# Performance work log

Measured on AMD Instinct MI355X. Metric: run time of the kernel, lower is better.

The kernel has to match this reference:

```python
import jax, jax.numpy as jnp
import numpy as np

B, INPUT_LEN, F_IN = 32, 4096, 256
N = B * INPUT_LEN          # 131072 total nodes in the flattened batch
E = 4_194_304              # ~avg degree 32
HID, OUT = 3, 1            # GCNConv(256->3) then GCNConv(3->1), per source code
PRED_LEN = 1024


def setup_inputs() -> dict:
    key = jax.random.key(0)
    k = jax.random.split(key, 5)
    node_features = jax.random.normal(k[0], (B, INPUT_LEN, F_IN), dtype=jnp.float32)
    # flattened, already-offset edge index (Batch.from_data_list result)
    edge_index = jax.random.randint(k[1], (2, E), 0, N, dtype=jnp.int32)
    W1 = jax.random.normal(k[2], (F_IN, HID), dtype=jnp.float32) / np.float32(np.sqrt(F_IN))
    b1 = jnp.zeros((HID,), dtype=jnp.float32)
    W2 = jax.random.normal(k[3], (HID, OUT), dtype=jnp.float32) / np.float32(np.sqrt(HID))
    b2 = jnp.zeros((OUT,), dtype=jnp.float32)
    return {"node_features": node_features, "W1": W1, "b1": b1, "W2": W2, "b2": b2,
            "edge_index": edge_index, "pred_len": PRED_LEN, "input_len": INPUT_LEN}


def _gcn_norm(edge_index, num_nodes, dtype):
    # PyG gcn_norm: add self-loops, deg over destination, symmetric deg^-1/2 norm
    loop = jnp.arange(num_nodes, dtype=edge_index.dtype)
    src = jnp.concatenate([edge_index[0], loop])
    dst = jnp.concatenate([edge_index[1], loop])
    deg = jax.ops.segment_sum(jnp.ones_like(src, dtype=dtype), dst, num_segments=num_nodes)
    dinv = jnp.where(deg > 0, jax.lax.rsqrt(deg), 0.0).astype(dtype)
    norm = dinv[src] * dinv[dst]  # [E+N]
    return src, dst, norm


def _gcn_conv(x, src, dst, norm, W, b, num_nodes):
    h = x @ W                              # [N, out] linear first (small out dim)
    msg = h[src] * norm[:, None]           # gather + scale per edge
    out = jax.ops.segment_sum(msg, dst, num_segments=num_nodes)  # scatter-add
    return out + b


def reference(node_features, W1, b1, W2, b2, edge_index, pred_len, input_len):
    n_nodes = node_features.shape[0] * node_features.shape[1]
    x = node_features.reshape(n_nodes, node_features.shape[2])
    src, dst, norm = _gcn_norm(edge_index, n_nodes, x.dtype)
    h = jax.nn.relu(_gcn_conv(x, src, dst, norm, W1, b1, n_nodes))
    h = _gcn_conv(h, src, dst, norm, W2, b2, n_nodes)
    h = h.reshape(-1, input_len, h.shape[1])   # [B, input_len, num_target]
    return h[:, :pred_len, :]
```

## Files before the change

### kernel.cpp

```cpp
#include <hip/hip_runtime.h>
#include <hip/hip_bf16.h>
#include <stdint.h>

#define F_IN 256
#define QSCALE 512.0f
#define QBIAS  8192
#define FMASK  0x1FFFFFull
#define H2Q    16384.0f
#define NBUK   16
#define BCAP   524288
#define LCAP   384
#define XBUF_SZ  (32u << 20)
#define DEGSTG_OFF (32u << 20)
#define STG1_OFF   (34u << 20)
#define STG2_OFF   (50u << 20)
#define SCRATCH_SZ (52u << 20)

__device__ __forceinline__ float bf2f(unsigned short u) {
    union { unsigned int i; float f; } v; v.i = ((unsigned int)u) << 16; return v.f;
}
__device__ __forceinline__ unsigned short f2bf(float f) {
    union { unsigned int i; float f; } v; v.f = f;
    unsigned int r = v.i + 0x7FFF + ((v.i >> 16) & 1);
    return (unsigned short)(r >> 16);
}
__device__ __forceinline__ unsigned long long packq(float v0, float v1, float v2) {
    int m0 = __float2int_rn(v0 * QSCALE);
    int m1 = __float2int_rn(v1 * QSCALE);
    int m2 = __float2int_rn(v2 * QSCALE);
    m0 = max(-4095, min(4095, m0));
    m1 = max(-4095, min(4095, m1));
    m2 = max(-4095, min(4095, m2));
    return (unsigned long long)(unsigned)(m0 + QBIAS)
         | ((unsigned long long)(unsigned)(m1 + QBIAS) << 21)
         | ((unsigned long long)(unsigned)(m2 + QBIAS) << 42);
}

__global__ void k_init(unsigned int* __restrict__ gcur,
                       const unsigned int* __restrict__ w1w, int* __restrict__ flag) {
    __shared__ int cnt;
    if (threadIdx.x == 0) cnt = 0;
    if (threadIdx.x < NBUK) gcur[threadIdx.x] = 0u;
    __syncthreads();
    int local = 0;
    for (int i = threadIdx.x; i < 384; i += blockDim.x) {
        unsigned e = (w1w[i] >> 7) & 0xFF;
        if (e >= 100 && e <= 135) local++;
    }
    atomicAdd(&cnt, local);
    __syncthreads();
    if (threadIdx.x == 0) *flag = (2 * cnt < 384) ? 1 : 0;
}

__global__ void __launch_bounds__(1024)
k_bucket(const int* __restrict__ src, const int* __restrict__ dst,
         unsigned int* __restrict__ xbuf, unsigned int* __restrict__ gcur, int E) {
    __shared__ unsigned int lbuf[NBUK][LCAP];
    __shared__ unsigned int lcnt[NBUK];
    __shared__ unsigned int lbase[NBUK];
    if (threadIdx.x < NBUK) lcnt[threadIdx.x] = 0u;
    __syncthreads();
    int g4 = blockIdx.x * 1024 + threadIdx.x;
    int4 s4 = ((const int4*)src)[g4];
    int4 d4 = ((const int4*)dst)[g4];
    #pragma unroll
    for (int u = 0; u < 4; u++) {
        int s = (u == 0) ? s4.x : (u == 1) ? s4.y : (u == 2) ? s4.z : s4.w;
        int d = (u == 0) ? d4.x : (u == 1) ? d4.y : (u == 2) ? d4.z : d4.w;
        unsigned p = ((unsigned)s << 13) | ((unsigned)d & 8191u);
        int bk = ((unsigned)d) >> 13;
        unsigned lp = atomicAdd(&lcnt[bk], 1u);
        if (lp < LCAP) lbuf[bk][lp] = p;
        else {
            unsigned g = atomicAdd(&gcur[bk], 1u);
            xbuf[(size_t)bk * BCAP + g] = p;
        }
    }
    __syncthreads();
    if (threadIdx.x < NBUK) {
        unsigned c = min(lcnt[threadIdx.x], (unsigned)LCAP);
        lcnt[threadIdx.x] = c;
        lbase[threadIdx.x] = atomicAdd(&gcur[threadIdx.x], c);
    }
    __syncthreads();
    for (int bk = 0; bk < NBUK; bk++) {
        unsigned c = lcnt[bk], base = lbase[bk];
        for (unsigned i = threadIdx.x; i < c; i += 1024)
            xbuf[(size_t)bk * BCAP + base + i] = lbuf[bk][i];
    }
}

__global__ void __launch_bounds__(1024)
k_gemv_bhist(int bhistB,
             const unsigned int* __restrict__ xbuf, const unsigned int* __restrict__ gcur,
             unsigned int* __restrict__ degstg,
             const void* __restrict__ xv_, const void* __restrict__ w1_,
             unsigned short* __restrict__ h1con,
             const int* __restrict__ flag, int N) {
    __shared__ unsigned int cnt8[2048];
    int b = blockIdx.x;
    if (b < bhistB) {
        int bucket = b & 15, sub = b >> 4;
        for (int i = threadIdx.x; i < 2048; i += 1024) cnt8[i] = 0u;
        __syncthreads();
        unsigned cnt = gcur[bucket];
        unsigned e0 = (unsigned)(((unsigned long long)sub       * cnt) >> 4);
        unsigned e1 = (unsigned)(((unsigned long long)(sub + 1) * cnt) >> 4);
        const unsigned int* bp = xbuf + (size_t)bucket * BCAP;
        for (unsigned i = e0 + threadIdx.x; i < e1; i += 1024) {
            unsigned q = bp[i] & 8191u;
            atomicAdd(&cnt8[q >> 2], 1u << ((q & 3u) << 3));
        }
        __syncthreads();
        unsigned int* out = degstg + (size_t)b * 2048;
        for (int i = threadIdx.x; i < 2048; i += 1024) out[i] = cnt8[i];
        return;
    }
    int wave = threadIdx.x >> 6;
    int lane = threadIdx.x & 63;
    int row0 = ((b - bhistB) * 16 + wave) * 2;
    if (row0 >= N) return;
    int f32mode = *flag;

    float xa0, xa1, xa2, xa3, xb0, xb1, xb2, xb3;
    float w00, w01, w02, w10, w11, w12, w20, w21, w22, w30, w31, w32;
    if (f32mode) {
        const float4* xra = (const float4*)((const float*)xv_ + (size_t)row0 * F_IN);
        const float4* xrb = (const float4*)((const float*)xv_ + (size_t)(row0 + 1) * F_IN);
        float4 va = xra[lane], vb = xrb[lane];
        xa0 = va.x; xa1 = va.y; xa2 = va.z; xa3 = va.w;
        xb0 = vb.x; xb1 = vb.y; xb2 = vb.z; xb3 = vb.w;
        const float4* wr = (const float4*)w1_;
        float4 wa = wr[lane*3+0], wb = wr[lane*3+1], wc = wr[lane*3+2];
        w00 = wa.x; w01 = wa.y; w02 = wa.z; w10 = wa.w;
        w11 = wb.x; w12 = wb.y; w20 = wb.z; w21 = wb.w;
        w22 = wc.x; w30 = wc.y; w31 = wc.z; w32 = wc.w;
    } else {
        const ushort4* xra = (const ushort4*)((const unsigned short*)xv_ + (size_t)row0 * F_IN);
        const ushort4* xrb = (const ushort4*)((const unsigned short*)xv_ + (size_t)(row0 + 1) * F_IN);
        ushort4 va = xra[lane], vb = xrb[lane];
        xa0 = bf2f(va.x); xa1 = bf2f(va.y); xa2 = bf2f(va.z); xa3 = bf2f(va.w);
        xb0 = bf2f(vb.x); xb1 = bf2f(vb.y); xb2 = bf2f(vb.z); xb3 = bf2f(vb.w);
        const ushort4* wr = (const ushort4*)w1_;
        ushort4 wa = wr[lane*3+0], wb = wr[lane*3+1], wc = wr[lane*3+2];
        w00 = bf2f(wa.x); w01 = bf2f(wa.y); w02 = bf2f(wa.z); w10 = bf2f(wa.w);
        w11 = bf2f(wb.x); w12 = bf2f(wb.y); w20 = bf2f(wb.z); w21 = bf2f(wb.w);
        w22 = bf2f(wc.x); w30 = bf2f(wc.y); w31 = bf2f(wc.z); w32 = bf2f(wc.w);
    }
    float pa0 = xa0*w00 + xa1*w10 + xa2*w20 + xa3*w30;
    float pa1 = xa0*w01 + xa1*w11 + xa2*w21 + xa3*w31;
    float pa2 = xa0*w02 + xa1*w12 + xa2*w22 + xa3*w32;
    float pb0 = xb0*w00 + xb1*w10 + xb2*w20 + xb3*w30;
    float pb1 = xb0*w01 + xb1*w11 + xb2*w21 + xb3*w31;
    float pb2 = xb0*w02 + xb1*w12 + xb2*w22 + xb3*w32;
    #pragma unroll
    for (int off = 32; off; off >>= 1) {
        pa0 += __shfl_down(pa0, off, 64);
        pa1 += __shfl_down(pa1, off, 64);
        pa2 += __shfl_down(pa2, off, 64);
        pb0 += __shfl_down(pb0, off, 64);
        pb1 += __shfl_down(pb1, off, 64);
        pb2 += __shfl_down(pb2, off, 64);
    }
    if (lane == 0) {
        ushort4 oa, ob;
        oa.x = f2bf(pa0); oa.y = f2bf(pa1); oa.z = f2bf(pa2); oa.w = 0;
        ob.x = f2bf(pb0); ob.y = f2bf(pb1); ob.z = f2bf(pb2); ob.w = 0;
        ((ushort4*)h1con)[row0]     = oa;
        ((ushort4*)h1con)[row0 + 1] = ob;
    }
}

__global__ void k_dinvpack(const unsigned char* __restrict__ degstg,
                           unsigned char* __restrict__ deg8, float* __restrict__ dinv,
                           unsigned long long* __restrict__ h1con, int N) {
    int n = blockIdx.x * blockDim.x + threadIdx.x;
    if (n >= N) return;
    int bk = n >> 13, idx = n & 8191;
    unsigned deg = 1u;
    #pragma unroll
    for (int s = 0; s < 16; s++)
        deg += degstg[(size_t)((s << 4) | bk) * 8192 + idx];
    deg8[n] = (unsigned char)deg;
    float dv = rsqrtf((float)deg);
    dinv[n] = dv;
    ushort4 h = ((const ushort4*)h1con)[n];
    h1con[n] = packq(bf2f(h.x) * dv, bf2f(h.y) * dv, bf2f(h.z) * dv);
}

__global__ void __launch_bounds__(1024)
k_scatter1(const unsigned int* __restrict__ xbuf,
           const unsigned long long* __restrict__ con,
           unsigned long long* __restrict__ stg1,
           const unsigned int* __restrict__ gcur) {
    __shared__ unsigned long long acc[8192];
    int bucket = blockIdx.x & 15, sub = blockIdx.x >> 4;
    for (int i = threadIdx.x; i < 8192; i += 1024) acc[i] = 0ull;
    __syncthreads();
    unsigned cnt = gcur[bucket];
    unsigned e0 = (unsigned)(((unsigned long long)sub       * cnt) >> 4);
    unsigned e1 = (unsigned)(((unsigned long long)(sub + 1) * cnt) >> 4);
    const unsigned int* bp = xbuf + (size_t)bucket * BCAP;
    for (unsigned i = e0 + threadIdx.x; i < e1; i += 1024) {
        unsigned p = bp[i];
        atomicAdd(&acc[p & 8191u], con[p >> 13]);
    }
    __syncthreads();
    unsigned long long* out = stg1 + (size_t)blockIdx.x * 8192;
    for (int i = threadIdx.x; i < 8192; i += 1024) out[i] = acc[i];
}

__global__ void k_rlin2(const unsigned long long* __restrict__ stg1,
                        const unsigned long long* __restrict__ con,
                        const unsigned char* __restrict__ deg8,
                        const float* __restrict__ dinv,
                        const void* __restrict__ b1_, const void* __restrict__ w2_,
                        int* __restrict__ h2q, const int* __restrict__ flag, int N) {
    int n = blockIdx.x * blockDim.x + threadIdx.x;
    if (n >= N) return;
    int f32mode = *flag;
    float b10, b11, b12, w20, w21, w22;
    if (f32mode) {
        const float* b1 = (const float*)b1_; const float* w2 = (const float*)w2_;
        b10 = b1[0]; b11 = b1[1]; b12 = b1[2];
        w20 = w2[0]; w21 = w2[1]; w22 = w2[2];
    } else {
        const unsigned short* b1 = (const unsigned short*)b1_;
        const unsigned short* w2 = (const unsigned short*)w2_;
        b10 = bf2f(b1[0]); b11 = bf2f(b1[1]); b12 = bf2f(b1[2]);
        w20 = bf2f(w2[0]); w21 = bf2f(w2[1]); w22 = bf2f(w2[2]);
    }
    int bk = n >> 13, idx = n & 8191;
    unsigned long long T = con[n];
    #pragma unroll
    for (int s = 0; s < 16; s++)
        T += stg1[(size_t)((s << 4) | bk) * 8192 + idx];
    long long dbias = (long long)deg8[n] * QBIAS;
    float q = 1.0f / QSCALE;
    float s0 = (float)((long long)( T        & FMASK) - dbias) * q;
    float s1 = (float)((long long)((T >> 21) & FMASK) - dbias) * q;
    float s2 = (float)((long long)((T >> 42) & FMASK) - dbias) * q;
    float dv = dinv[n];
    float a0 = fmaxf(s0 * dv + b10, 0.0f);
    float a1 = fmaxf(s1 * dv + b11, 0.0f);
    float a2 = fmaxf(s2 * dv + b12, 0.0f);
    float h2 = (a0 * w20 + a1 * w21 + a2 * w22) * dv;
    h2q[n] = __float2int_rn(h2 * H2Q);
}

__global__ void __launch_bounds__(1024)
k_scatter2(const unsigned int* __restrict__ xbuf, const int* __restrict__ h2q,
           int* __restrict__ stg2, const unsigned int* __restrict__ gcur) {
    __shared__ int acc[2048];
    int bucket = blockIdx.x & 15, sub = blockIdx.x >> 4;
    for (int i = threadIdx.x; i < 2048; i += 1024) acc[i] = 0;
    __syncthreads();
    unsigned cnt = gcur[bucket];
    unsigned e0 = (unsigned)(((unsigned long long)sub       * cnt) >> 4);
    unsigned e1 = (unsigned)(((unsigned long long)(sub + 1) * cnt) >> 4);
    const unsigned int* bp = xbuf + (size_t)bucket * BCAP;
    for (unsigned i = e0 + threadIdx.x; i < e1; i += 1024) {
        unsigned p = bp[i];
        unsigned low = p & 8191u;
        if ((low & 4095u) < 1024u) {
            int cl = (int)(((low >> 12) << 10) | (low & 1023u));
            atomicAdd(&acc[cl], h2q[p >> 13]);
        }
    }
    __syncthreads();
    int* out = stg2 + (size_t)blockIdx.x * 2048;
    for (int i = threadIdx.x; i < 2048; i += 1024) out[i] = acc[i];
}

__global__ void k_r2out(const int* __restrict__ stg2, const int* __restrict__ h2q,
                        const float* __restrict__ dinv, const void* __restrict__ b2_,
                        void* __restrict__ out_, const int* __restrict__ flag, int M) {
    int t = blockIdx.x * blockDim.x + threadIdx.x;
    if (t >= M) return;
    int f32mode = *flag;
    float b2 = f32mode ? ((const float*)b2_)[0] : bf2f(((const unsigned short*)b2_)[0]);
    int n = ((t >> 10) << 12) | (t & 1023);
    int bk = n >> 13;
    unsigned low = (unsigned)n & 8191u;
    int cl = (int)(((low >> 12) << 10) | (low & 1023u));
    int S = h2q[n];
    #pragma unroll
    for (int s = 0; s < 16; s++)
        S += stg2[(size_t)((s << 4) | bk) * 2048 + cl];
    float v = (float)S * (1.0f / H2Q) * dinv[n] + b2;
    if (f32mode) ((float*)out_)[t] = v;
    else         ((unsigned short*)out_)[t] = f2bf(v);
}

extern "C" void kernel_launch(void* const* d_in, const int* in_sizes, int n_in,
                              void* d_out, int out_size, void* d_ws, size_t ws_size,
                              hipStream_t stream) {
    void*       x   = d_in[0];
    const void* w1  = d_in[1];
    const void* b1  = d_in[2];
    const void* w2  = d_in[3];
    const void* b2  = d_in[4];
    const int* eidx = (const int*)d_in[5];

    const int N = in_sizes[0] / F_IN;
    const int E = in_sizes[5] / 2;
    const int* src = eidx;
    const int* dst = eidx + E;

    char* ws = (char*)d_ws;
    unsigned char*      deg8  = (unsigned char*)(ws);
    float*              dinv  = (float*)(ws + (size_t)N);
    unsigned long long* h1con = (unsigned long long*)(ws + (size_t)5*N);
    int*                h2q   = (int*)(ws + (size_t)13*N);
    int*                flag  = (int*)(ws + (size_t)17*N);
    unsigned int*       gcur  = (unsigned int*)(ws + (size_t)17*N + 64);

    bool big_ws = ws_size >= ((size_t)(4u << 20) + SCRATCH_SZ);
    char* scratch = big_ws ? (ws + (4u << 20)) : (char*)x;
    unsigned int*       xbuf   = (unsigned int*)scratch;
    unsigned int*       degstg = (unsigned int*)(scratch + DEGSTG_OFF);
    unsigned long long* stg1   = (unsigned long long*)(scratch + STG1_OFF);
    int*                stg2   = (int*)(scratch + STG2_OFF);

    const int bs = 256;
    int gemvB = N / 32;
    k_init<<<1, bs, 0, stream>>>(gcur, (const unsigned int*)w1, flag);
    if (big_ws) {
        k_bucket<<<E / 4096, 1024, 0, stream>>>(src, dst, xbuf, gcur, E);
        k_gemv_bhist<<<256 + gemvB, 1024, 0, stream>>>(256, xbuf, gcur, degstg,
                                                       x, w1, (unsigned short*)h1con,
                                                       flag, N);
    } else {
        k_gemv_bhist<<<gemvB, 1024, 0, stream>>>(0, nullptr, gcur, degstg,
                                                 x, w1, (unsigned short*)h1con,
                                                 flag, N);
        k_bucket<<<E / 4096, 1024, 0, stream>>>(src, dst, xbuf, gcur, E);
        k_gemv_bhist<<<256, 1024, 0, stream>>>(256, xbuf, gcur, degstg,
                                               x, w1, (unsigned short*)h1con,
                                               flag, N);
    }
    k_dinvpack<<<(N + bs-1)/bs, bs, 0, stream>>>((const unsigned char*)degstg,
                                                 deg8, dinv, h1con, N);
    k_scatter1<<<256, 1024, 0, stream>>>(xbuf, h1con, stg1, gcur);
    k_rlin2   <<<(N + bs-1)/bs, bs, 0, stream>>>(stg1, h1con, deg8, dinv, b1, w2,
                                                 h2q, flag, N);
    k_scatter2<<<256, 1024, 0, stream>>>(xbuf, h2q, stg2, gcur);
    k_r2out   <<<(out_size + bs-1)/bs, bs, 0, stream>>>(stg2, h2q, dinv, b2,
                                                        d_out, flag, out_size);
}
```

Baseline: 283.3 us.

## Use 256 fine-grained buckets so each block owns its destination range, fusing reductions

Edges are binned into 256 buckets of 512 destination nodes instead of 16 buckets of 8192. Each block can then hold a whole bucket's accumulators in shared memory, so the per-sub-block staging buffers and the separate reduction kernels (dinvpack, rlin2, r2out) go away and are fused into the histogram and scatter kernels. The bucketing pass is also merged with the GEMV in one launch, and the final scatter only processes buckets that hold predicted outputs. The trade-off is only 256 blocks per scatter pass with lower parallelism per bucket, tiny local buffers with more global atomics for overflow, and silent truncation if a bucket exceeds its capacity.

```diff
diff --git a/kernel.cpp b/kernel.cpp
--- a/kernel.cpp
+++ b/kernel.cpp
@@ -1,5 +1,4 @@
 #include <hip/hip_runtime.h>
-#include <hip/hip_bf16.h>
 #include <stdint.h>
 
 #define F_IN 256
@@ -7,14 +6,14 @@
 #define QBIAS  8192
 #define FMASK  0x1FFFFFull
 #define H2Q    16384.0f
-#define NBUK   16
-#define BCAP   524288
-#define LCAP   384
-#define XBUF_SZ  (32u << 20)
-#define DEGSTG_OFF (32u << 20)
-#define STG1_OFF   (34u << 20)
-#define STG2_OFF   (50u << 20)
-#define SCRATCH_SZ (52u << 20)
+#define NBUK   256
+#define BSH    9
+#define BMASK  511u
+#define BCAP   32768
+#define BCSH   15
+#define LCAP   56
+#define EPB    8192
+#define XBUF_SZ ((size_t)NBUK * BCAP * 4)
 
 __device__ __forceinline__ float bf2f(unsigned short u) {
     union { unsigned int i; float f; } v; v.i = ((unsigned int)u) << 16; return v.f;
@@ -40,7 +39,7 @@
                        const unsigned int* __restrict__ w1w, int* __restrict__ flag) {
     __shared__ int cnt;
     if (threadIdx.x == 0) cnt = 0;
-    if (threadIdx.x < NBUK) gcur[threadIdx.x] = 0u;
+    for (int i = threadIdx.x; i < NBUK * 16; i += blockDim.x) gcur[i] = 0u;
     __syncthreads();
     int local = 0;
     for (int i = threadIdx.x; i < 384; i += blockDim.x) {
@@ -53,72 +52,55 @@
 }
 
 __global__ void __launch_bounds__(1024)
-k_bucket(const int* __restrict__ src, const int* __restrict__ dst,
-         unsigned int* __restrict__ xbuf, unsigned int* __restrict__ gcur, int E) {
+k_bucket_gemv(int bucketB,
+              const int* __restrict__ src, const int* __restrict__ dst,
+              unsigned int* __restrict__ xbuf, unsigned int* __restrict__ gcur,
+              const void* __restrict__ xv_, const void* __restrict__ w1_,
+              unsigned short* __restrict__ h1out,
+              const int* __restrict__ flag, int N) {
     __shared__ unsigned int lbuf[NBUK][LCAP];
     __shared__ unsigned int lcnt[NBUK];
     __shared__ unsigned int lbase[NBUK];
-    if (threadIdx.x < NBUK) lcnt[threadIdx.x] = 0u;
-    __syncthreads();
-    int g4 = blockIdx.x * 1024 + threadIdx.x;
-    int4 s4 = ((const int4*)src)[g4];
-    int4 d4 = ((const int4*)dst)[g4];
-    #pragma unroll
-    for (int u = 0; u < 4; u++) {
-        int s = (u == 0) ? s4.x : (u == 1) ? s4.y : (u == 2) ? s4.z : s4.w;
-        int d = (u == 0) ? d4.x : (u == 1) ? d4.y : (u == 2) ? d4.z : d4.w;
-        unsigned p = ((unsigned)s << 13) | ((unsigned)d & 8191u);
-        int bk = ((unsigned)d) >> 13;
-        unsigned lp = atomicAdd(&lcnt[bk], 1u);
-        if (lp < LCAP) lbuf[bk][lp] = p;
-        else {
-            unsigned g = atomicAdd(&gcur[bk], 1u);
-            xbuf[(size_t)bk * BCAP + g] = p;
-        }
-    }
-    __syncthreads();
-    if (threadIdx.x < NBUK) {
-        unsigned c = min(lcnt[threadIdx.x], (unsigned)LCAP);
-        lcnt[threadIdx.x] = c;
-        lbase[threadIdx.x] = atomicAdd(&gcur[threadIdx.x], c);
-    }
-    __syncthreads();
-    for (int bk = 0; bk < NBUK; bk++) {
-        unsigned c = lcnt[bk], base = lbase[bk];
-        for (unsigned i = threadIdx.x; i < c; i += 1024)
-            xbuf[(size_t)bk * BCAP + base + i] = lbuf[bk][i];
-    }
-}
-
-__global__ void __launch_bounds__(1024)
-k_gemv_bhist(int bhistB,
-             const unsigned int* __restrict__ xbuf, const unsigned int* __restrict__ gcur,
-             unsigned int* __restrict__ degstg,
-             const void* __restrict__ xv_, const void* __restrict__ w1_,
-             unsigned short* __restrict__ h1con,
-             const int* __restrict__ flag, int N) {
-    __shared__ unsigned int cnt8[2048];
     int b = blockIdx.x;
-    if (b < bhistB) {
-        int bucket = b & 15, sub = b >> 4;
-        for (int i = threadIdx.x; i < 2048; i += 1024) cnt8[i] = 0u;
+    if (b < bucketB) {
+        for (int i = threadIdx.x; i < NBUK; i += 1024) lcnt[i] = 0u;
         __syncthreads();
-        unsigned cnt = gcur[bucket];
-        unsigned e0 = (unsigned)(((unsigned long long)sub       * cnt) >> 4);
-        unsigned e1 = (unsigned)(((unsigned long long)(sub + 1) * cnt) >> 4);
-        const unsigned int* bp = xbuf + (size_t)bucket * BCAP;
-        for (unsigned i = e0 + threadIdx.x; i < e1; i += 1024) {
-            unsigned q = bp[i] & 8191u;
-            atomicAdd(&cnt8[q >> 2], 1u << ((q & 3u) << 3));
+        int g4 = b * 2048 + threadIdx.x;
+        int4 sa = ((const int4*)src)[g4];
+        int4 da = ((const int4*)dst)[g4];
+        int4 sb = ((const int4*)src)[g4 + 1024];
+        int4 db = ((const int4*)dst)[g4 + 1024];
+        int ss[8] = {sa.x, sa.y, sa.z, sa.w, sb.x, sb.y, sb.z, sb.w};
+        int dd[8] = {da.x, da.y, da.z, da.w, db.x, db.y, db.z, db.w};
+        #pragma unroll
+        for (int u = 0; u < 8; u++) {
+            unsigned p = ((unsigned)ss[u] << BSH) | ((unsigned)dd[u] & BMASK);
+            int bk = ((unsigned)dd[u]) >> BSH;
+            unsigned lp = atomicAdd(&lcnt[bk], 1u);
+            if (lp < LCAP) lbuf[bk][lp] = p;
+            else {
+                unsigned g = atomicAdd(&gcur[bk << 4], 1u);
+                if (g < BCAP) xbuf[((size_t)bk << BCSH) + g] = p;
+            }
         }
         __syncthreads();
-        unsigned int* out = degstg + (size_t)b * 2048;
-        for (int i = threadIdx.x; i < 2048; i += 1024) out[i] = cnt8[i];
+        if (threadIdx.x < NBUK) {
+            unsigned c = min(lcnt[threadIdx.x], (unsigned)LCAP);
+            lcnt[threadIdx.x] = c;
+            lbase[threadIdx.x] = atomicAdd(&gcur[threadIdx.x << 4], c);
+        }
+        __syncthreads();
+        int wave = threadIdx.x >> 6, lane = threadIdx.x & 63;
+        for (int bk = wave * 16; bk < wave * 16 + 16; bk++) {
+            unsigned c = lcnt[bk], base = lbase[bk];
+            for (unsigned i = lane; i < c; i += 64)
+                xbuf[((size_t)bk << BCSH) + base + i] = lbuf[bk][i];
+        }
         return;
     }
     int wave = threadIdx.x >> 6;
     int lane = threadIdx.x & 63;
-    int row0 = ((b - bhistB) * 16 + wave) * 2;
+    int row0 = ((b - bucketB) * 16 + wave) * 2;
     if (row0 >= N) return;
     int f32mode = *flag;
 
@@ -166,130 +148,109 @@
         ushort4 oa, ob;
         oa.x = f2bf(pa0); oa.y = f2bf(pa1); oa.z = f2bf(pa2); oa.w = 0;
         ob.x = f2bf(pb0); ob.y = f2bf(pb1); ob.z = f2bf(pb2); ob.w = 0;
-        ((ushort4*)h1con)[row0]     = oa;
-        ((ushort4*)h1con)[row0 + 1] = ob;
-    }
-}
-
-__global__ void k_dinvpack(const unsigned char* __restrict__ degstg,
-                           unsigned char* __restrict__ deg8, float* __restrict__ dinv,
-                           unsigned long long* __restrict__ h1con, int N) {
-    int n = blockIdx.x * blockDim.x + threadIdx.x;
-    if (n >= N) return;
-    int bk = n >> 13, idx = n & 8191;
-    unsigned deg = 1u;
-    #pragma unroll
-    for (int s = 0; s < 16; s++)
-        deg += degstg[(size_t)((s << 4) | bk) * 8192 + idx];
-    deg8[n] = (unsigned char)deg;
-    float dv = rsqrtf((float)deg);
-    dinv[n] = dv;
-    ushort4 h = ((const ushort4*)h1con)[n];
-    h1con[n] = packq(bf2f(h.x) * dv, bf2f(h.y) * dv, bf2f(h.z) * dv);
+        ((ushort4*)h1out)[row0]     = oa;
+        ((ushort4*)h1out)[row0 + 1] = ob;
+    }
 }
 
 __global__ void __launch_bounds__(1024)
-k_scatter1(const unsigned int* __restrict__ xbuf,
-           const unsigned long long* __restrict__ con,
-           unsigned long long* __restrict__ stg1,
-           const unsigned int* __restrict__ gcur) {
-    __shared__ unsigned long long acc[8192];
-    int bucket = blockIdx.x & 15, sub = blockIdx.x >> 4;
-    for (int i = threadIdx.x; i < 8192; i += 1024) acc[i] = 0ull;
-    __syncthreads();
-    unsigned cnt = gcur[bucket];
-    unsigned e0 = (unsigned)(((unsigned long long)sub       * cnt) >> 4);
-    unsigned e1 = (unsigned)(((unsigned long long)(sub + 1) * cnt) >> 4);
-    const unsigned int* bp = xbuf + (size_t)bucket * BCAP;
-    for (unsigned i = e0 + threadIdx.x; i < e1; i += 1024) {
+k_hist_pack(const unsigned int* __restrict__ xbuf, const unsigned int* __restrict__ gcur,
+            unsigned char* __restrict__ deg8, float* __restrict__ dinv,
+            unsigned long long* __restrict__ h1con) {
+    __shared__ unsigned int cnt[512];
+    int B = blockIdx.x;
+    for (int i = threadIdx.x; i < 512; i += 1024) cnt[i] = 0u;
+    __syncthreads();
+    unsigned ce = min(gcur[B << 4], (unsigned)BCAP);
+    const unsigned int* bp = xbuf + ((size_t)B << BCSH);
+    for (unsigned i = threadIdx.x; i < ce; i += 1024)
+        atomicAdd(&cnt[bp[i] & BMASK], 1u);
+    __syncthreads();
+    if (threadIdx.x < 512) {
+        int n = (B << BSH) | threadIdx.x;
+        unsigned deg = 1u + cnt[threadIdx.x];
+        deg8[n] = (unsigned char)min(deg, 255u);
+        float dv = rsqrtf((float)deg);
+        dinv[n] = dv;
+        ushort4 h = ((const ushort4*)h1con)[n];
+        h1con[n] = packq(bf2f(h.x) * dv, bf2f(h.y) * dv, bf2f(h.z) * dv);
+    }
+}
+
+__global__ void __launch_bounds__(1024)
+k_scat1_lin2(const unsigned int* __restrict__ xbuf, const unsigned int* __restrict__ gcur,
+             const unsigned long long* __restrict__ con,
+             const unsigned char* __restrict__ deg8, const float* __restrict__ dinv,
+             const void* __restrict__ b1_, const void* __restrict__ w2_,
+             int* __restrict__ h2q, const int* __restrict__ flag) {
+    __shared__ unsigned long long acc[512];
+    int B = blockIdx.x;
+    for (int i = threadIdx.x; i < 512; i += 1024) acc[i] = 0ull;
+    __syncthreads();
+    unsigned ce = min(gcur[B << 4], (unsigned)BCAP);
+    const unsigned int* bp = xbuf + ((size_t)B << BCSH);
+    for (unsigned i = threadIdx.x; i < ce; i += 1024) {
         unsigned p = bp[i];
-        atomicAdd(&acc[p & 8191u], con[p >> 13]);
-    }
-    __syncthreads();
-    unsigned long long* out = stg1 + (size_t)blockIdx.x * 8192;
-    for (int i = threadIdx.x; i < 8192; i += 1024) out[i] = acc[i];
-}
-
-__global__ void k_rlin2(const unsigned long long* __restrict__ stg1,
-                        const unsigned long long* __restrict__ con,
-                        const unsigned char* __restrict__ deg8,
-                        const float* __restrict__ dinv,
-                        const void* __restrict__ b1_, const void* __restrict__ w2_,
-                        int* __restrict__ h2q, const int* __restrict__ flag, int N) {
-    int n = blockIdx.x * blockDim.x + threadIdx.x;
-    if (n >= N) return;
-    int f32mode = *flag;
-    float b10, b11, b12, w20, w21, w22;
-    if (f32mode) {
-        const float* b1 = (const float*)b1_; const float* w2 = (const float*)w2_;
-        b10 = b1[0]; b11 = b1[1]; b12 = b1[2];
-        w20 = w2[0]; w21 = w2[1]; w22 = w2[2];
-    } else {
-        const unsigned short* b1 = (const unsigned short*)b1_;
-        const unsigned short* w2 = (const unsigned short*)w2_;
-        b10 = bf2f(b1[0]); b11 = bf2f(b1[1]); b12 = bf2f(b1[2]);
-        w20 = bf2f(w2[0]); w21 = bf2f(w2[1]); w22 = bf2f(w2[2]);
-    }
-    int bk = n >> 13, idx = n & 8191;
-    unsigned long long T = con[n];
-    #pragma unroll
-    for (int s = 0; s < 16; s++)
-        T += stg1[(size_t)((s << 4) | bk) * 8192 + idx];
-    long long dbias = (long long)deg8[n] * QBIAS;
-    float q = 1.0f / QSCALE;
-    float s0 = (float)((long long)( T        & FMASK) - dbias) * q;
-    float s1 = (float)((long long)((T >> 21) & FMASK) - dbias) * q;
-    float s2 = (float)((long long)((T >> 42) & FMASK) - dbias) * q;
-    float dv = dinv[n];
-    float a0 = fmaxf(s0 * dv + b10, 0.0f);
-    float a1 = fmaxf(s1 * dv + b11, 0.0f);
-    float a2 = fmaxf(s2 * dv + b12, 0.0f);
-    float h2 = (a0 * w20 + a1 * w21 + a2 * w22) * dv;
-    h2q[n] = __float2int_rn(h2 * H2Q);
+        atomicAdd(&acc[p & BMASK], con[p >> BSH]);
+    }
+    __syncthreads();
+    if (threadIdx.x < 512) {
+        int n = (B << BSH) | threadIdx.x;
+        int f32mode = *flag;
+        float b10, b11, b12, w20, w21, w22;
+        if (f32mode) {
+            const float* b1 = (const float*)b1_; const float* w2 = (const float*)w2_;
+            b10 = b1[0]; b11 = b1[1]; b12 = b1[2];
+            w20 = w2[0]; w21 = w2[1]; w22 = w2[2];
+        } else {
+            const unsigned short* b1 = (const unsigned short*)b1_;
+            const unsigned short* w2 = (const unsigned short*)w2_;
+            b10 = bf2f(b1[0]); b11 = bf2f(b1[1]); b12 = bf2f(b1[2]);
+            w20 = bf2f(w2[0]); w21 = bf2f(w2[1]); w22 = bf2f(w2[2]);
+        }
+        unsigned long long T = acc[threadIdx.x] + con[n];
+        long long dbias = (long long)deg8[n] * QBIAS;
+        float q = 1.0f / QSCALE;
+        float s0 = (float)((long long)( T        & FMASK) - dbias) * q;
+        float s1 = (float)((long long)((T >> 21) & FMASK) - dbias) * q;
+        float s2 = (float)((long long)((T >> 42) & FMASK) - dbias) * q;
+        float dv = dinv[n];
+        float a0 = fmaxf(s0 * dv + b10, 0.0f);
+        float a1 = fmaxf(s1 * dv + b11, 0.0f);
+        float a2 = fmaxf(s2 * dv + b12, 0.0f);
+        float h2 = (a0 * w20 + a1 * w21 + a2 * w22) * dv;
+        h2q[n] = __float2int_rn(h2 * H2Q);
+    }
 }
 
 __global__ void __launch_bounds__(1024)
-k_scatter2(const unsigned int* __restrict__ xbuf, const int* __restrict__ h2q,
-           int* __restrict__ stg2, const unsigned int* __restrict__ gcur) {
-    __shared__ int acc[2048];
-    int bucket = blockIdx.x & 15, sub = blockIdx.x >> 4;
-    for (int i = threadIdx.x; i < 2048; i += 1024) acc[i] = 0;
-    __syncthreads();
-    unsigned cnt = gcur[bucket];
-    unsigned e0 = (unsigned)(((unsigned long long)sub       * cnt) >> 4);
-    unsigned e1 = (unsigned)(((unsigned long long)(sub + 1) * cnt) >> 4);
-    const unsigned int* bp = xbuf + (size_t)bucket * BCAP;
-    for (unsigned i = e0 + threadIdx.x; i < e1; i += 1024) {
+k_scat2_out(const unsigned int* __restrict__ xbuf, const unsigned int* __restrict__ gcur,
+            const int* __restrict__ h2q, const float* __restrict__ dinv,
+            const void* __restrict__ b2_, void* __restrict__ out_,
+            const int* __restrict__ flag) {
+    __shared__ int acc[512];
+    int ob = blockIdx.x;
+    int B = ((ob >> 1) << 3) | (ob & 1);
+    for (int i = threadIdx.x; i < 512; i += 1024) acc[i] = 0;
+    __syncthreads();
+    unsigned ce = min(gcur[B << 4], (unsigned)BCAP);
+    const unsigned int* bp = xbuf + ((size_t)B << BCSH);
+    for (unsigned i = threadIdx.x; i < ce; i += 1024) {
         unsigned p = bp[i];
-        unsigned low = p & 8191u;
-        if ((low & 4095u) < 1024u) {
-            int cl = (int)(((low >> 12) << 10) | (low & 1023u));
-            atomicAdd(&acc[cl], h2q[p >> 13]);
-        }
-    }
-    __syncthreads();
-    int* out = stg2 + (size_t)blockIdx.x * 2048;
-    for (int i = threadIdx.x; i < 2048; i += 1024) out[i] = acc[i];
-}
-
-__global__ void k_r2out(const int* __restrict__ stg2, const int* __restrict__ h2q,
-                        const float* __restrict__ dinv, const void* __restrict__ b2_,
-                        void* __restrict__ out_, const int* __restrict__ flag, int M) {
-    int t = blockIdx.x * blockDim.x + threadIdx.x;
-    if (t >= M) return;
-    int f32mode = *flag;
-    float b2 = f32mode ? ((const float*)b2_)[0] : bf2f(((const unsigned short*)b2_)[0]);
-    int n = ((t >> 10) << 12) | (t & 1023);
-    int bk = n >> 13;
-    unsigned low = (unsigned)n & 8191u;
-    int cl = (int)(((low >> 12) << 10) | (low & 1023u));
-    int S = h2q[n];
-    #pragma unroll
-    for (int s = 0; s < 16; s++)
-        S += stg2[(size_t)((s << 4) | bk) * 2048 + cl];
-    float v = (float)S * (1.0f / H2Q) * dinv[n] + b2;
-    if (f32mode) ((float*)out_)[t] = v;
-    else         ((unsigned short*)out_)[t] = f2bf(v);
+        atomicAdd(&acc[p & BMASK], h2q[p >> BSH]);
+    }
+    __syncthreads();
+    if (threadIdx.x < 512) {
+        int i = threadIdx.x;
+        int n = (B << BSH) | i;
+        int f32mode = *flag;
+        float b2 = f32mode ? ((const float*)b2_)[0] : bf2f(((const unsigned short*)b2_)[0]);
+        int S = h2q[n] + acc[i];
+        float v = (float)S * (1.0f / H2Q) * dinv[n] + b2;
+        int t = ((B >> 3) << 10) | ((B & 1) << 9) | i;
+        if (f32mode) ((float*)out_)[t] = v;
+        else         ((unsigned short*)out_)[t] = f2bf(v);
+    }
 }
 
 extern "C" void kernel_launch(void* const* d_in, const int* in_sizes, int n_in,
@@ -315,36 +276,27 @@
     int*                flag  = (int*)(ws + (size_t)17*N);
     unsigned int*       gcur  = (unsigned int*)(ws + (size_t)17*N + 64);
 
-    bool big_ws = ws_size >= ((size_t)(4u << 20) + SCRATCH_SZ);
-    char* scratch = big_ws ? (ws + (4u << 20)) : (char*)x;
-    unsigned int*       xbuf   = (unsigned int*)scratch;
-    unsigned int*       degstg = (unsigned int*)(scratch + DEGSTG_OFF);
-    unsigned long long* stg1   = (unsigned long long*)(scratch + STG1_OFF);
-    int*                stg2   = (int*)(scratch + STG2_OFF);
-
-    const int bs = 256;
-    int gemvB = N / 32;
-    k_init<<<1, bs, 0, stream>>>(gcur, (const unsigned int*)w1, flag);
+    bool big_ws = ws_size >= ((size_t)(4u << 20) + XBUF_SZ);
+    unsigned int* xbuf = (unsigned int*)(big_ws ? (ws + (4u << 20)) : (char*)x);
+
+    int bucketB = E / EPB;
+    int gemvB   = N / 32;
+    k_init<<<1, 256, 0, stream>>>(gcur, (const unsigned int*)w1, flag);
     if (big_ws) {
-        k_bucket<<<E / 4096, 1024, 0, stream>>>(src, dst, xbuf, gcur, E);
-        k_gemv_bhist<<<256 + gemvB, 1024, 0, stream>>>(256, xbuf, gcur, degstg,
-                                                       x, w1, (unsigned short*)h1con,
-                                                       flag, N);
+        k_bucket_gemv<<<bucketB + gemvB, 1024, 0, stream>>>(bucketB, src, dst,
+                                                            xbuf, gcur, x, w1,
+                                                            (unsigned short*)h1con,
+                                                            flag, N);
     } else {
-        k_gemv_bhist<<<gemvB, 1024, 0, stream>>>(0, nullptr, gcur, degstg,
-                                                 x, w1, (unsigned short*)h1con,
-                                                 flag, N);
-        k_bucket<<<E / 4096, 1024, 0, stream>>>(src, dst, xbuf, gcur, E);
-        k_gemv_bhist<<<256, 1024, 0, stream>>>(256, xbuf, gcur, degstg,
-                                               x, w1, (unsigned short*)h1con,
-                                               flag, N);
-    }
-    k_dinvpack<<<(N + bs-1)/bs, bs, 0, stream>>>((const unsigned char*)degstg,
-                                                 deg8, dinv, h1con, N);
-    k_scatter1<<<256, 1024, 0, stream>>>(xbuf, h1con, stg1, gcur);
-    k_rlin2   <<<(N + bs-1)/bs, bs, 0, stream>>>(stg1, h1con, deg8, dinv, b1, w2,
-                                                 h2q, flag, N);
-    k_scatter2<<<256, 1024, 0, stream>>>(xbuf, h2q, stg2, gcur);
-    k_r2out   <<<(out_size + bs-1)/bs, bs, 0, stream>>>(stg2, h2q, dinv, b2,
-                                                        d_out, flag, out_size);
-}
+        k_bucket_gemv<<<gemvB, 1024, 0, stream>>>(0, src, dst, xbuf, gcur,
+                                                  x, w1, (unsigned short*)h1con,
+                                                  flag, N);
+        k_bucket_gemv<<<bucketB, 1024, 0, stream>>>(bucketB, src, dst, xbuf, gcur,
+                                                    x, w1, (unsigned short*)h1con,
+                                                    flag, N);
+    }
+    k_hist_pack  <<<NBUK, 1024, 0, stream>>>(xbuf, gcur, deg8, dinv, h1con);
+    k_scat1_lin2 <<<NBUK, 1024, 0, stream>>>(xbuf, gcur, h1con, deg8, dinv,
+                                             b1, w2, h2q, flag);
+    k_scat2_out  <<<64, 1024, 0, stream>>>(xbuf, gcur, h2q, dinv, b2, d_out, flag);
+}
```

After: 285.6 us. No clear change (+0.8%).
